# Optimization experiments

Measured on AMD Instinct MI355X. Metric: run time of the kernel, lower is better.

The kernel has to match this reference:

```python
import jax, jax.numpy as jnp
import numpy as np

B, T, D, H = 2, 2048, 768, 12
HS = D // H


def setup_inputs() -> dict:
    key = jax.random.key(0)
    ks = jax.random.split(key, 11)
    s = 1.0 / np.sqrt(D)
    return {
        "query": jax.random.normal(ks[0], (B, T, D), jnp.float32),
        "key": jax.random.normal(ks[1], (B, T, D), jnp.float32),
        "value": jax.random.normal(ks[2], (B, T, D), jnp.float32),
        "Wq": jax.random.normal(ks[3], (D, D), jnp.float32) * s,
        "bq": jax.random.normal(ks[4], (D,), jnp.float32) * s,
        "Wk": jax.random.normal(ks[5], (D, D), jnp.float32) * s,
        "bk": jax.random.normal(ks[6], (D,), jnp.float32) * s,
        "Wv": jax.random.normal(ks[7], (D, D), jnp.float32) * s,
        "bv": jax.random.normal(ks[8], (D,), jnp.float32) * s,
        "Wo": jax.random.normal(ks[9], (D, D), jnp.float32) * s,
        "bo": jax.random.normal(ks[10], (D,), jnp.float32) * s,
    }


def reference(query, key, value, Wq, bq, Wk, bk, Wv, bv, Wo, bo):
    # Projections (torch nn.Linear: x @ W.T + b), then split heads -> [B,H,T,HS]
    def split_heads(x):
        return x.reshape(B, -1, H, HS).transpose(0, 2, 1, 3)

    q = split_heads(query @ Wq.T + bq)
    k = split_heads(key @ Wk.T + bk)
    v = split_heads(value @ Wv.T + bv)

    scale = 1.0 / jnp.sqrt(jnp.asarray(HS, q.dtype))
    scores = jnp.einsum("bhqd,bhkd->bhqk", q, k) * scale  # [B,H,Tq,Tk]
    attn = jax.nn.softmax(scores, axis=-1)
    out = jnp.einsum("bhqk,bhkd->bhqd", attn, v)  # [B,H,Tq,HS]
    out = out.transpose(0, 2, 1, 3).reshape(B, -1, D)
    output = out @ Wo.T + bo
    return output, attn.mean(axis=1)
```

## Files before the change

### kernel.cpp

```cpp
#include <hip/hip_runtime.h>
#include <hip/hip_fp16.h>
#include <stdint.h>

typedef _Float16 f16;
typedef _Float16 f16x8 __attribute__((ext_vector_type(8)));
typedef _Float16 f16x4v __attribute__((ext_vector_type(4)));
typedef __fp16 h16x2 __attribute__((ext_vector_type(2)));
typedef float f32x4 __attribute__((ext_vector_type(4)));
typedef float f32x16 __attribute__((ext_vector_type(16)));

#define MFMA32(a,b,c) __builtin_amdgcn_mfma_f32_32x32x16_f16(a,b,c,0,0,0)
#define CVTPK(a,b) __builtin_amdgcn_cvt_pkrtz(a,b)

#if __has_builtin(__builtin_amdgcn_exp2f)
#define EXP2(x) __builtin_amdgcn_exp2f(x)
#else
#define EXP2(x) exp2f(x)
#endif

static __device__ __forceinline__ float dot2acc(h16x2 a, float c) {
#if __has_builtin(__builtin_amdgcn_fdot2)
    const h16x2 one = { (__fp16)1.f, (__fp16)1.f };
    return __builtin_amdgcn_fdot2(a, one, c, false);
#else
    return c + (float)a[0] + (float)a[1];
#endif
}

typedef __attribute__((address_space(1))) void gvoid_t;
typedef __attribute__((address_space(3))) void svoid_t;
#define AS1(p) ((gvoid_t*)(uintptr_t)(p))
#define AS3(p) ((svoid_t*)(uint32_t)(uintptr_t)(p))

static constexpr int Bc = 2, Tc = 2048, Dc = 768, Hc = 12;
static constexpr int Mc = Bc * Tc;
static constexpr float SC2 = 0.18033688011112042f;

union PA { f16x8 v; h16x2 h[4]; };

#define FRAG32(BASE, ROWOFF, CHUNK) \
    (*(const f16x8*)((const char*)(BASE) + \
        ((ROWOFF) + q32) * 128 + (((CHUNK) ^ g7) * 16)))

#define FRAGP(BASE, ROWOFF, C) \
    (*(const f16x8*)((const char*)(BASE) + \
        (((ROWOFF) / 2 + (q32 >> 1)) * 128) + \
        (((((q32 & 1) << 2) | (C)) ^ ((q32 >> 1) & 7)) * 16)))

__global__ __launch_bounds__(256) void conv_all(
    const float* __restrict__ q, const float* __restrict__ k, const float* __restrict__ v,
    const float* __restrict__ wq, const float* __restrict__ wk, const float* __restrict__ wv,
    const float* __restrict__ wo,
    f16* __restrict__ qh, f16* __restrict__ kh, f16* __restrict__ vh,
    f16* __restrict__ wqh, f16* __restrict__ wkh, f16* __restrict__ wvh, f16* __restrict__ woh)
{
    const int NI = (Mc * Dc) / 4;
    const int NW = (Dc * Dc) / 4;
    int i = blockIdx.x * 256 + threadIdx.x;
    if (i >= 3 * NI + 4 * NW) return;
    const float4* src; f16* dst; int j; float scl = 1.f;
    if (i < 3 * NI) {
        int a = i / NI; j = i - a * NI;
        src = (const float4*)(a == 0 ? q : (a == 1 ? k : v));
        dst = (a == 0 ? qh : (a == 1 ? kh : vh));
    } else {
        int t = i - 3 * NI;
        int a = t / NW; j = t - a * NW;
        src = (const float4*)(a == 0 ? wq : (a == 1 ? wk : (a == 2 ? wv : wo)));
        dst = (a == 0 ? wqh : (a == 1 ? wkh : (a == 2 ? wvh : woh)));
        if (a == 0) scl = SC2;
    }
    float4 f = src[j];
    f16x4v o = { (f16)(f.x * scl), (f16)(f.y * scl), (f16)(f.z * scl), (f16)(f.w * scl) };
    *(f16x4v*)(dst + 4 * j) = o;
}

__device__ __forceinline__ void gemm_bk32(
    const f16* __restrict__ A, const f16* __restrict__ W,
    int brow, int bcol, char* As, char* Bs, f32x16 acc[2])
{
    const int tid = threadIdx.x;
    const int w = tid >> 6, lane = tid & 63;
    const int q32 = lane & 31, hi = lane >> 5;
    const int wr = w >> 1, wc = w & 1;
    const int wbase16 = (tid & ~63) * 16;

#define GSA(KT_, BUF_) do { \
    const int k0_ = (KT_) * 32; \
    _Pragma("unroll") \
    for (int j_ = 0; j_ < 2; ++j_) { \
        const int p_ = j_ * 256 + tid; \
        const int L_ = p_ >> 3, c8_ = (p_ & 7) ^ (L_ & 7); \
        const int row_ = 2 * L_ + (c8_ >> 2), kc_ = (c8_ & 3) * 8; \
        __builtin_amdgcn_global_load_lds(AS1(A + (size_t)(brow + row_) * 768 + k0_ + kc_), \
            AS3(As + (BUF_) * 8192 + j_ * 4096 + wbase16), 16, 0, 0); \
    } } while (0)
#define GSB(KT_, BUF_) do { \
    const int k0_ = (KT_) * 32; \
    const int L_ = tid >> 3, c8_ = (tid & 7) ^ (L_ & 7); \
    const int row_ = 2 * L_ + (c8_ >> 2), kc_ = (c8_ & 3) * 8; \
    __builtin_amdgcn_global_load_lds(AS1(W + (size_t)(bcol + row_) * 768 + k0_ + kc_), \
        AS3(Bs + (BUF_) * 4096 + wbase16), 16, 0, 0); \
    } while (0)

    GSA(0, 0); GSB(0, 0);
    __syncthreads();
    for (int kt = 0; kt < 24; ++kt) {
        const int cur = kt & 1;
        if (kt < 23) { GSA(kt + 1, cur ^ 1); GSB(kt + 1, cur ^ 1); }
        const char* As_ = As + cur * 8192;
        const char* Bs_ = Bs + cur * 4096;
#pragma unroll
        for (int ks = 0; ks < 2; ++ks) {
            const f16x8 af0 = FRAGP(As_, wr * 64,      ks * 2 + hi);
            const f16x8 af1 = FRAGP(As_, wr * 64 + 32, ks * 2 + hi);
            const f16x8 bf  = FRAGP(Bs_, wc * 32,      ks * 2 + hi);
            acc[0] = MFMA32(af0, bf, acc[0]);
            acc[1] = MFMA32(af1, bf, acc[1]);
        }
        __syncthreads();
    }
#undef GSA
#undef GSB
}

__global__ __launch_bounds__(256) void qkv_proj(
    const f16* __restrict__ qh, const f16* __restrict__ kh, const f16* __restrict__ vh,
    const f16* __restrict__ wqh, const f16* __restrict__ wkh, const f16* __restrict__ wvh,
    const float* __restrict__ bq, const float* __restrict__ bk, const float* __restrict__ bv,
    f16* __restrict__ Qp, f16* __restrict__ Kp, f16* __restrict__ Vt)
{
    __shared__ char lds[24576];
    char* As = lds; char* Bs = lds + 16384;

    const int z = blockIdx.z;
    const f16* A = (z == 0) ? qh : (z == 1) ? kh : vh;
    const f16* W = (z == 0) ? wqh : (z == 1) ? wkh : wvh;
    const float* bias = (z == 0) ? bq : (z == 1) ? bk : bv;
    const int brow = blockIdx.y * 128, bcol = blockIdx.x * 64;

    f32x16 acc[2];
#pragma unroll
    for (int mi = 0; mi < 2; ++mi)
#pragma unroll
        for (int r = 0; r < 16; ++r) acc[mi][r] = 0.f;

    gemm_bk32(A, W, brow, bcol, As, Bs, acc);

    const int tid = threadIdx.x, w = tid >> 6, lane = tid & 63;
    const int q32 = lane & 31, hi = lane >> 5;
    const int wr = w >> 1, wc = w & 1;
    const int c = bcol + wc * 32 + q32;
    const float bval = (z == 0) ? bias[c] * SC2 : bias[c];

    if (z < 2) {
        f16* dst = (z == 0) ? Qp : Kp;
#pragma unroll
        for (int mi = 0; mi < 2; ++mi)
#pragma unroll
            for (int r = 0; r < 16; ++r) {
                const int row = brow + wr * 64 + mi * 32 + (r & 3) + 8 * (r >> 2) + 4 * hi;
                dst[(size_t)row * 768 + c] = (f16)(acc[mi][r] + bval);
            }
    } else {
        __syncthreads();
        const int dl = wc * 32 + q32;
#pragma unroll
        for (int mi = 0; mi < 2; ++mi)
#pragma unroll
            for (int j = 0; j < 8; ++j) {
                const int r0 = 2 * j;
                const int crow = (r0 & 3) + 8 * (r0 >> 2) + 4 * hi;
                const int sw = ((crow >> 2) ^ (crow >> 3)) & 1;
                const int tp = crow ^ (sw * 12);
                const int tloc = wr * 64 + mi * 32 + tp;
                const h16x2 pv = CVTPK(acc[mi][r0] + bval, acc[mi][r0 + 1] + bval);
                *(h16x2*)(As + dl * 256 + ((tloc * 2) ^ ((dl & 7) << 4))) = pv;
            }
        __syncthreads();
        const int bb = brow >> 11, t0 = brow & 2047, hh = bcol >> 6;
        f16* Vh = Vt + ((size_t)(bb * 12 + hh) * 64) * 2048;
#pragma unroll
        for (int j = 0; j < 4; ++j) {
            const int dr = j * 16 + (tid >> 4), off = tid & 15;
            const f16x8 vv = *(const f16x8*)(As + dr * 256 + ((off * 16) ^ ((dr & 7) << 4)));
            *(f16x8*)(Vh + (size_t)dr * 2048 + t0 + off * 8) = vv;
        }
    }
}

__global__ __launch_bounds__(256, 3) void attn_out(
    const f16* __restrict__ Qp, const f16* __restrict__ Kp, const f16* __restrict__ Vt,
    float* __restrict__ l_inv, f16* __restrict__ ctx)
{
    __shared__ f16 Kbuf[2][4096];
    __shared__ f16 Vbuf[2][4096];
    __shared__ float Ored[2][32][64];
    __shared__ float lred[2][2][32];

    const int qt = blockIdx.x, h = blockIdx.y, b = blockIdx.z;
    const int tid = threadIdx.x, w = tid >> 6, lane = tid & 63;
    const int q32 = lane & 31, hi = lane >> 5, g7 = lane & 7;
    const int qh = w & 1, kh = w >> 1;
    const int wbase16 = (tid & ~63) * 16;

    const size_t qrow0 = (size_t)b * 2048 + qt * 64 + qh * 32;
    const int hcol = h * 64;

    const f16* qb = Qp + (qrow0 + q32) * 768 + hcol + hi * 8;
    f16x8 bqf[4];
#pragma unroll
    for (int d = 0; d < 4; ++d) bqf[d] = *(const f16x8*)(qb + d * 16);

    const size_t kbase = (size_t)b * 2048;
    const f16* Vg = Vt + ((size_t)(b * 12 + h)) * 64 * 2048;

    f32x16 oacc[2];
#pragma unroll
    for (int dt = 0; dt < 2; ++dt)
#pragma unroll
        for (int r = 0; r < 16; ++r) oacc[dt][r] = 0.f;
    float lsum = 0.f;

#define STAGE_KV(KT_, BUF) do { \
    _Pragma("unroll") \
    for (int j_ = 0; j_ < 2; ++j_) { \
        const int p_ = j_ * 256 + tid; \
        const int row_ = p_ >> 3, c_ = (p_ & 7) ^ (row_ & 7); \
        __builtin_amdgcn_global_load_lds( \
            AS1(Kp + (kbase + (size_t)(KT_) * 64 + row_) * 768 + hcol + c_ * 8), \
            AS3((char*)&Kbuf[BUF][0] + j_ * 4096 + wbase16), 16, 0, 0); \
        __builtin_amdgcn_global_load_lds( \
            AS1(Vg + (size_t)row_ * 2048 + (KT_) * 64 + c_ * 8), \
            AS3((char*)&Vbuf[BUF][0] + j_ * 4096 + wbase16), 16, 0, 0); \
    } } while (0)

#define AOBODY(CUR) do { \
    const f16* Kb_ = &Kbuf[CUR][0]; const f16* Vb_ = &Vbuf[CUR][0]; \
    f32x16 sa; \
    _Pragma("unroll") \
    for (int r_ = 0; r_ < 16; ++r_) sa[r_] = 0.f; \
    sa = MFMA32(FRAG32(Kb_, kh * 32, 0 + hi), bqf[0], sa); \
    sa = MFMA32(FRAG32(Kb_, kh * 32, 2 + hi), bqf[1], sa); \
    sa = MFMA32(FRAG32(Kb_, kh * 32, 4 + hi), bqf[2], sa); \
    sa = MFMA32(FRAG32(Kb_, kh * 32, 6 + hi), bqf[3], sa); \
    float p[16]; \
    _Pragma("unroll") \
    for (int r_ = 0; r_ < 16; ++r_) p[r_] = EXP2(sa[r_]); \
    PA pa0, pa1; \
    pa0.h[0] = CVTPK(p[0], p[1]);   pa0.h[1] = CVTPK(p[2], p[3]); \
    pa0.h[2] = CVTPK(p[4], p[5]);   pa0.h[3] = CVTPK(p[6], p[7]); \
    pa1.h[0] = CVTPK(p[8], p[9]);   pa1.h[1] = CVTPK(p[10], p[11]); \
    pa1.h[2] = CVTPK(p[12], p[13]); pa1.h[3] = CVTPK(p[14], p[15]); \
    float t0_ = 0.f, t1_ = 0.f; \
    t0_ = dot2acc(pa0.h[0], t0_); t0_ = dot2acc(pa0.h[1], t0_); \
    t0_ = dot2acc(pa0.h[2], t0_); t0_ = dot2acc(pa0.h[3], t0_); \
    t1_ = dot2acc(pa1.h[0], t1_); t1_ = dot2acc(pa1.h[1], t1_); \
    t1_ = dot2acc(pa1.h[2], t1_); t1_ = dot2acc(pa1.h[3], t1_); \
    lsum += t0_ + t1_; \
    oacc[0] = MFMA32(FRAG32(Vb_, 0,  kh * 4 + 0 + hi), pa0.v, oacc[0]); \
    oacc[0] = MFMA32(FRAG32(Vb_, 0,  kh * 4 + 2 + hi), pa1.v, oacc[0]); \
    oacc[1] = MFMA32(FRAG32(Vb_, 32, kh * 4 + 0 + hi), pa0.v, oacc[1]); \
    oacc[1] = MFMA32(FRAG32(Vb_, 32, kh * 4 + 2 + hi), pa1.v, oacc[1]); \
} while (0)

    STAGE_KV(0, 0);
    __syncthreads();
    for (int kt = 0; kt < 32; ++kt) {
        const int cur = kt & 1;
        if (kt < 31) STAGE_KV(kt + 1, cur ^ 1);
        AOBODY(cur);
        __syncthreads();
    }
#undef STAGE_KV
#undef AOBODY

    lsum += __shfl_xor(lsum, 32);
    if (hi == 0) lred[kh][qh][q32] = lsum;
    if (kh == 1) {
#pragma unroll
        for (int dt = 0; dt < 2; ++dt)
#pragma unroll
            for (int g = 0; g < 4; ++g) {
                float4 v4 = { oacc[dt][g * 4 + 0], oacc[dt][g * 4 + 1],
                              oacc[dt][g * 4 + 2], oacc[dt][g * 4 + 3] };
                *(float4*)&Ored[qh][q32][dt * 32 + g * 8 + hi * 4] = v4;
            }
    }
    __syncthreads();
    if (kh == 0) {
        const float iv = 1.f / (lred[0][qh][q32] + lred[1][qh][q32]);
        if (hi == 0)
            l_inv[((size_t)(b * 12 + h)) * 2048 + qt * 64 + qh * 32 + q32] = iv;
        f16* cb = ctx + (qrow0 + q32) * 768 + hcol;
#pragma unroll
        for (int dt = 0; dt < 2; ++dt)
#pragma unroll
            for (int g = 0; g < 4; ++g) {
                const int d0 = dt * 32 + g * 8 + hi * 4;
                const float4 o4 = *(const float4*)&Ored[qh][q32][d0];
                f16x4v s;
#pragma unroll
                for (int e = 0; e < 4; ++e)
                    s[e] = (f16)((oacc[dt][g * 4 + e] + (&o4.x)[e]) * iv);
                *(f16x4v*)(cb + d0) = s;
            }
    }
}

__global__ __launch_bounds__(256) void tail_fused(
    const f16* __restrict__ ctx, const f16* __restrict__ woh,
    const float* __restrict__ bo, float* __restrict__ out,
    const f16* __restrict__ Qp, const f16* __restrict__ Kp,
    const float* __restrict__ l_inv, float* __restrict__ om)
{
    __shared__ char sh[32768];

    const int tid = threadIdx.x, w = tid >> 6, lane = tid & 63;
    const int q32 = lane & 31, hi = lane >> 5, g7 = lane & 7;
    const int wbase16 = (tid & ~63) * 16;

    if (blockIdx.x < 384) {
        const int brow = (blockIdx.x / 12) * 128, bcol = (blockIdx.x % 12) * 64;
        f32x16 acc[2];
#pragma unroll
        for (int mi = 0; mi < 2; ++mi)
#pragma unroll
            for (int r = 0; r < 16; ++r) acc[mi][r] = 0.f;

        gemm_bk32(ctx, woh, brow, bcol, sh, sh + 16384, acc);

        const int wr = w >> 1, wc = w & 1;
        const int c = bcol + wc * 32 + q32;
        const float bval = bo[c];
#pragma unroll
        for (int mi = 0; mi < 2; ++mi)
#pragma unroll
            for (int r = 0; r < 16; ++r) {
                const int row = brow + wr * 64 + mi * 32 + (r & 3) + 8 * (r >> 2) + 4 * hi;
                out[(size_t)row * 768 + c] = acc[mi][r] + bval;
            }
    } else {
        const int mb = blockIdx.x - 384;
        const int kt = mb & 31, r2 = mb >> 5;
        const int qt = r2 & 31, b = r2 >> 5;
        const int qh = w & 1, kh = w >> 1;

        char* Qb = sh;
        char* Kb = sh + 16384;

        const size_t qtrow = (size_t)b * 2048 + qt * 64;
        const size_t ktrow = (size_t)b * 2048 + kt * 64;

        f32x16 macc;
#pragma unroll
        for (int r = 0; r < 16; ++r) macc[r] = 0.f;

#define MSTAGE(H_, BUF) do { \
    _Pragma("unroll") \
    for (int j_ = 0; j_ < 2; ++j_) { \
        const int p_ = j_ * 256 + tid; \
        const int row_ = p_ >> 3, c_ = (p_ & 7) ^ (row_ & 7); \
        __builtin_amdgcn_global_load_lds( \
            AS1(Qp + (qtrow + row_) * 768 + (H_) * 64 + c_ * 8), \
            AS3(Qb + (BUF) * 8192 + j_ * 4096 + wbase16), 16, 0, 0); \
        __builtin_amdgcn_global_load_lds( \
            AS1(Kp + (ktrow + row_) * 768 + (H_) * 64 + c_ * 8), \
            AS3(Kb + (BUF) * 8192 + j_ * 4096 + wbase16), 16, 0, 0); \
    } } while (0)

#define MBODY(H_, CUR) do { \
    const f16* Qb_ = (const f16*)(Qb + (CUR) * 8192); \
    const f16* Kb_ = (const f16*)(Kb + (CUR) * 8192); \
    f16x8 qf[4]; \
    _Pragma("unroll") \
    for (int d_ = 0; d_ < 4; ++d_) qf[d_] = FRAG32(Qb_, qh * 32, d_ * 2 + hi); \
    f32x16 sa; \
    _Pragma("unroll") \
    for (int r_ = 0; r_ < 16; ++r_) sa[r_] = 0.f; \
    sa = MFMA32(FRAG32(Kb_, kh * 32, 0 + hi), qf[0], sa); \
    sa = MFMA32(FRAG32(Kb_, kh * 32, 2 + hi), qf[1], sa); \
    sa = MFMA32(FRAG32(Kb_, kh * 32, 4 + hi), qf[2], sa); \
    sa = MFMA32(FRAG32(Kb_, kh * 32, 6 + hi), qf[3], sa); \
    const float ivv = l_inv[((size_t)(b * 12 + (H_))) * 2048 + qt * 64 + qh * 32 + q32]; \
    _Pragma("unroll") \
    for (int r_ = 0; r_ < 16; ++r_) macc[r_] += EXP2(sa[r_]) * ivv; \
} while (0)

        MSTAGE(0, 0);
        __syncthreads();
        for (int h = 0; h < 12; ++h) {
            const int cur = h & 1;
            if (h < 11) MSTAGE(h + 1, cur ^ 1);
            MBODY(h, cur);
            __syncthreads();
        }
#undef MSTAGE
#undef MBODY

        float* ob = om + ((size_t)(b * 2048 + qt * 64 + qh * 32 + q32)) * 2048
                  + kt * 64 + kh * 32;
#pragma unroll
        for (int g = 0; g < 4; ++g) {
            float4 v4 = { macc[g * 4 + 0] * (1.0f / 12.0f),
                          macc[g * 4 + 1] * (1.0f / 12.0f),
                          macc[g * 4 + 2] * (1.0f / 12.0f),
                          macc[g * 4 + 3] * (1.0f / 12.0f) };
            *(float4*)(ob + g * 8 + hi * 4) = v4;
        }
    }
}

extern "C" void kernel_launch(void* const* d_in, const int* in_sizes, int n_in,
                              void* d_out, int out_size, void* d_ws, size_t ws_size,
                              hipStream_t stream) {
    const float* q  = (const float*)d_in[0];
    const float* k  = (const float*)d_in[1];
    const float* v  = (const float*)d_in[2];
    const float* Wq = (const float*)d_in[3];
    const float* bq = (const float*)d_in[4];
    const float* Wk = (const float*)d_in[5];
    const float* bk = (const float*)d_in[6];
    const float* Wv = (const float*)d_in[7];
    const float* bv = (const float*)d_in[8];
    const float* Wo = (const float*)d_in[9];
    const float* bo = (const float*)d_in[10];
    float* out = (float*)d_out;

    char* ws = (char*)d_ws;
    const size_t SZ_IN = (size_t)Mc * Dc * 2;
    const size_t SZ_W  = (size_t)Dc * Dc * 2;
    f16* qh  = (f16*)(ws);
    f16* kh  = (f16*)(ws + SZ_IN);
    f16* vh  = (f16*)(ws + 2 * SZ_IN);
    f16* wqh = (f16*)(ws + 3 * SZ_IN);
    f16* wkh = (f16*)(ws + 3 * SZ_IN + SZ_W);
    f16* wvh = (f16*)(ws + 3 * SZ_IN + 2 * SZ_W);
    f16* woh = (f16*)(ws + 3 * SZ_IN + 3 * SZ_W);
    f16* Qp  = (f16*)(ws + 3 * SZ_IN + 4 * SZ_W);
    f16* Kp  = (f16*)(ws + 4 * SZ_IN + 4 * SZ_W);
    f16* Vt  = (f16*)(ws + 5 * SZ_IN + 4 * SZ_W);
    f16* ctx = qh;
    float* l_inv = (float*)kh;

    conv_all<<<dim3(11520), dim3(256), 0, stream>>>(q, k, v, Wq, Wk, Wv, Wo,
                                                    qh, kh, vh, wqh, wkh, wvh, woh);
    qkv_proj<<<dim3(12, 32, 3), dim3(256), 0, stream>>>(qh, kh, vh, wqh, wkh, wvh,
                                                        bq, bk, bv, Qp, Kp, Vt);
    attn_out<<<dim3(32, 12, 2), dim3(256), 0, stream>>>(Qp, Kp, Vt, l_inv, ctx);
    tail_fused<<<dim3(2432), dim3(256), 0, stream>>>(ctx, woh, bo, out,
                                                     Qp, Kp, l_inv,
                                                     out + (size_t)Mc * Dc);
}
```

Measured before the change: 130.0 us.

## Fuse fp32-to-fp16 conversion into GEMM loaders, drop separate conversion kernel

The standalone conversion kernel that cast inputs and weights to fp16 is removed. The QKV projection GEMM now loads fp32 activations and weights into registers, converts them (applying the Q scale to Wq), and writes fp16 tiles to LDS. The output-projection GEMM does the same for Wo while still streaming ctx through direct global-to-LDS loads. This saves a kernel launch and the extra global write and read of fp16 copies. In exchange, each block reads twice the bytes per tile, weights are converted redundantly across blocks, and register-staged loads replace the async LDS path.

```diff
diff --git a/kernel.cpp b/kernel.cpp
--- a/kernel.cpp
+++ b/kernel.cpp
@@ -47,36 +47,9 @@
         (((ROWOFF) / 2 + (q32 >> 1)) * 128) + \
         (((((q32 & 1) << 2) | (C)) ^ ((q32 >> 1) & 7)) * 16)))
 
-__global__ __launch_bounds__(256) void conv_all(
-    const float* __restrict__ q, const float* __restrict__ k, const float* __restrict__ v,
-    const float* __restrict__ wq, const float* __restrict__ wk, const float* __restrict__ wv,
-    const float* __restrict__ wo,
-    f16* __restrict__ qh, f16* __restrict__ kh, f16* __restrict__ vh,
-    f16* __restrict__ wqh, f16* __restrict__ wkh, f16* __restrict__ wvh, f16* __restrict__ woh)
-{
-    const int NI = (Mc * Dc) / 4;
-    const int NW = (Dc * Dc) / 4;
-    int i = blockIdx.x * 256 + threadIdx.x;
-    if (i >= 3 * NI + 4 * NW) return;
-    const float4* src; f16* dst; int j; float scl = 1.f;
-    if (i < 3 * NI) {
-        int a = i / NI; j = i - a * NI;
-        src = (const float4*)(a == 0 ? q : (a == 1 ? k : v));
-        dst = (a == 0 ? qh : (a == 1 ? kh : vh));
-    } else {
-        int t = i - 3 * NI;
-        int a = t / NW; j = t - a * NW;
-        src = (const float4*)(a == 0 ? wq : (a == 1 ? wk : (a == 2 ? wv : wo)));
-        dst = (a == 0 ? wqh : (a == 1 ? wkh : (a == 2 ? wvh : woh)));
-        if (a == 0) scl = SC2;
-    }
-    float4 f = src[j];
-    f16x4v o = { (f16)(f.x * scl), (f16)(f.y * scl), (f16)(f.z * scl), (f16)(f.w * scl) };
-    *(f16x4v*)(dst + 4 * j) = o;
-}
-
-__device__ __forceinline__ void gemm_bk32(
-    const f16* __restrict__ A, const f16* __restrict__ W,
+template<bool AF32>
+__device__ __forceinline__ void gemm_bk32_t(
+    const void* Av, const float* __restrict__ W, float wscl,
     int brow, int bcol, char* As, char* Bs, f32x16 acc[2])
 {
     const int tid = threadIdx.x;
@@ -85,48 +58,89 @@
     const int wr = w >> 1, wc = w & 1;
     const int wbase16 = (tid & ~63) * 16;
 
-#define GSA(KT_, BUF_) do { \
-    const int k0_ = (KT_) * 32; \
+    int arow[2], akc[2];
+#pragma unroll
+    for (int j = 0; j < 2; ++j) {
+        const int p = j * 256 + tid;
+        const int L = p >> 3, c8 = (p & 7) ^ (L & 7);
+        arow[j] = 2 * L + (c8 >> 2); akc[j] = (c8 & 3) * 8;
+    }
+    const int bL = tid >> 3, bc8 = (tid & 7) ^ (bL & 7);
+    const int browW = 2 * bL + (bc8 >> 2), bkc = (bc8 & 3) * 8;
+
+    float4 af[2][2], bw[2];
+
+#define LOADW(KT_) do { \
+    const float* wp_ = W + (size_t)(bcol + browW) * 768 + (KT_) * 32 + bkc; \
+    bw[0] = *(const float4*)(wp_); bw[1] = *(const float4*)(wp_ + 4); } while (0)
+
+#define LOADA(KT_) do { \
     _Pragma("unroll") \
     for (int j_ = 0; j_ < 2; ++j_) { \
-        const int p_ = j_ * 256 + tid; \
-        const int L_ = p_ >> 3, c8_ = (p_ & 7) ^ (L_ & 7); \
-        const int row_ = 2 * L_ + (c8_ >> 2), kc_ = (c8_ & 3) * 8; \
-        __builtin_amdgcn_global_load_lds(AS1(A + (size_t)(brow + row_) * 768 + k0_ + kc_), \
-            AS3(As + (BUF_) * 8192 + j_ * 4096 + wbase16), 16, 0, 0); \
-    } } while (0)
-#define GSB(KT_, BUF_) do { \
-    const int k0_ = (KT_) * 32; \
-    const int L_ = tid >> 3, c8_ = (tid & 7) ^ (L_ & 7); \
-    const int row_ = 2 * L_ + (c8_ >> 2), kc_ = (c8_ & 3) * 8; \
-    __builtin_amdgcn_global_load_lds(AS1(W + (size_t)(bcol + row_) * 768 + k0_ + kc_), \
-        AS3(Bs + (BUF_) * 4096 + wbase16), 16, 0, 0); \
-    } while (0)
-
-    GSA(0, 0); GSB(0, 0);
+        const float* ap_ = (const float*)Av + (size_t)(brow + arow[j_]) * 768 + (KT_) * 32 + akc[j_]; \
+        af[j_][0] = *(const float4*)(ap_); af[j_][1] = *(const float4*)(ap_ + 4); } } while (0)
+
+#define GLDSA(KT_, BUF_) do { \
+    _Pragma("unroll") \
+    for (int j_ = 0; j_ < 2; ++j_) \
+        __builtin_amdgcn_global_load_lds( \
+            AS1((const f16*)Av + (size_t)(brow + arow[j_]) * 768 + (KT_) * 32 + akc[j_]), \
+            AS3(As + (BUF_) * 8192 + j_ * 4096 + wbase16), 16, 0, 0); } while (0)
+
+#define WRITEW(BUF_) do { \
+    f16x8 o_; \
+    _Pragma("unroll") \
+    for (int e_ = 0; e_ < 4; ++e_) o_[e_] = (f16)((&bw[0].x)[e_] * wscl); \
+    _Pragma("unroll") \
+    for (int e_ = 0; e_ < 4; ++e_) o_[4 + e_] = (f16)((&bw[1].x)[e_] * wscl); \
+    *(f16x8*)(Bs + (BUF_) * 4096 + tid * 16) = o_; } while (0)
+
+#define WRITEA(BUF_) do { \
+    _Pragma("unroll") \
+    for (int j_ = 0; j_ < 2; ++j_) { \
+        f16x8 o_; \
+        _Pragma("unroll") \
+        for (int e_ = 0; e_ < 4; ++e_) o_[e_] = (f16)((&af[j_][0].x)[e_]); \
+        _Pragma("unroll") \
+        for (int e_ = 0; e_ < 4; ++e_) o_[4 + e_] = (f16)((&af[j_][1].x)[e_]); \
+        *(f16x8*)(As + (BUF_) * 8192 + j_ * 4096 + tid * 16) = o_; } } while (0)
+
+    LOADW(0);
+    if constexpr (AF32) { LOADA(0); WRITEA(0); } else { GLDSA(0, 0); }
+    WRITEW(0);
     __syncthreads();
     for (int kt = 0; kt < 24; ++kt) {
         const int cur = kt & 1;
-        if (kt < 23) { GSA(kt + 1, cur ^ 1); GSB(kt + 1, cur ^ 1); }
+        if (kt < 23) {
+            LOADW(kt + 1);
+            if constexpr (AF32) LOADA(kt + 1); else GLDSA(kt + 1, cur ^ 1);
+        }
         const char* As_ = As + cur * 8192;
         const char* Bs_ = Bs + cur * 4096;
 #pragma unroll
         for (int ks = 0; ks < 2; ++ks) {
-            const f16x8 af0 = FRAGP(As_, wr * 64,      ks * 2 + hi);
-            const f16x8 af1 = FRAGP(As_, wr * 64 + 32, ks * 2 + hi);
-            const f16x8 bf  = FRAGP(Bs_, wc * 32,      ks * 2 + hi);
-            acc[0] = MFMA32(af0, bf, acc[0]);
-            acc[1] = MFMA32(af1, bf, acc[1]);
+            const f16x8 a0 = FRAGP(As_, wr * 64,      ks * 2 + hi);
+            const f16x8 a1 = FRAGP(As_, wr * 64 + 32, ks * 2 + hi);
+            const f16x8 bb = FRAGP(Bs_, wc * 32,      ks * 2 + hi);
+            acc[0] = MFMA32(a0, bb, acc[0]);
+            acc[1] = MFMA32(a1, bb, acc[1]);
+        }
+        if (kt < 23) {
+            if constexpr (AF32) WRITEA(cur ^ 1);
+            WRITEW(cur ^ 1);
         }
         __syncthreads();
     }
-#undef GSA
-#undef GSB
+#undef LOADW
+#undef LOADA
+#undef GLDSA
+#undef WRITEW
+#undef WRITEA
 }
 
 __global__ __launch_bounds__(256) void qkv_proj(
-    const f16* __restrict__ qh, const f16* __restrict__ kh, const f16* __restrict__ vh,
-    const f16* __restrict__ wqh, const f16* __restrict__ wkh, const f16* __restrict__ wvh,
+    const float* __restrict__ q, const float* __restrict__ k, const float* __restrict__ v,
+    const float* __restrict__ Wq, const float* __restrict__ Wk, const float* __restrict__ Wv,
     const float* __restrict__ bq, const float* __restrict__ bk, const float* __restrict__ bv,
     f16* __restrict__ Qp, f16* __restrict__ Kp, f16* __restrict__ Vt)
 {
@@ -134,9 +148,10 @@
     char* As = lds; char* Bs = lds + 16384;
 
     const int z = blockIdx.z;
-    const f16* A = (z == 0) ? qh : (z == 1) ? kh : vh;
-    const f16* W = (z == 0) ? wqh : (z == 1) ? wkh : wvh;
+    const float* A = (z == 0) ? q : (z == 1) ? k : v;
+    const float* W = (z == 0) ? Wq : (z == 1) ? Wk : Wv;
     const float* bias = (z == 0) ? bq : (z == 1) ? bk : bv;
+    const float wscl = (z == 0) ? SC2 : 1.f;
     const int brow = blockIdx.y * 128, bcol = blockIdx.x * 64;
 
     f32x16 acc[2];
@@ -145,7 +160,7 @@
 #pragma unroll
         for (int r = 0; r < 16; ++r) acc[mi][r] = 0.f;
 
-    gemm_bk32(A, W, brow, bcol, As, Bs, acc);
+    gemm_bk32_t<true>(A, W, wscl, brow, bcol, As, Bs, acc);
 
     const int tid = threadIdx.x, w = tid >> 6, lane = tid & 63;
     const int q32 = lane & 31, hi = lane >> 5;
@@ -309,7 +324,7 @@
 }
 
 __global__ __launch_bounds__(256) void tail_fused(
-    const f16* __restrict__ ctx, const f16* __restrict__ woh,
+    const f16* __restrict__ ctx, const float* __restrict__ Wo,
     const float* __restrict__ bo, float* __restrict__ out,
     const f16* __restrict__ Qp, const f16* __restrict__ Kp,
     const float* __restrict__ l_inv, float* __restrict__ om)
@@ -328,7 +343,7 @@
 #pragma unroll
             for (int r = 0; r < 16; ++r) acc[mi][r] = 0.f;
 
-        gemm_bk32(ctx, woh, brow, bcol, sh, sh + 16384, acc);
+        gemm_bk32_t<false>(ctx, Wo, 1.f, brow, bcol, sh, sh + 16384, acc);
 
         const int wr = w >> 1, wc = w & 1;
         const int c = bcol + wc * 32 + q32;
@@ -429,26 +444,16 @@
 
     char* ws = (char*)d_ws;
     const size_t SZ_IN = (size_t)Mc * Dc * 2;
-    const size_t SZ_W  = (size_t)Dc * Dc * 2;
-    f16* qh  = (f16*)(ws);
-    f16* kh  = (f16*)(ws + SZ_IN);
-    f16* vh  = (f16*)(ws + 2 * SZ_IN);
-    f16* wqh = (f16*)(ws + 3 * SZ_IN);
-    f16* wkh = (f16*)(ws + 3 * SZ_IN + SZ_W);
-    f16* wvh = (f16*)(ws + 3 * SZ_IN + 2 * SZ_W);
-    f16* woh = (f16*)(ws + 3 * SZ_IN + 3 * SZ_W);
-    f16* Qp  = (f16*)(ws + 3 * SZ_IN + 4 * SZ_W);
-    f16* Kp  = (f16*)(ws + 4 * SZ_IN + 4 * SZ_W);
-    f16* Vt  = (f16*)(ws + 5 * SZ_IN + 4 * SZ_W);
-    f16* ctx = qh;
-    float* l_inv = (float*)kh;
-
-    conv_all<<<dim3(11520), dim3(256), 0, stream>>>(q, k, v, Wq, Wk, Wv, Wo,
-                                                    qh, kh, vh, wqh, wkh, wvh, woh);
-    qkv_proj<<<dim3(12, 32, 3), dim3(256), 0, stream>>>(qh, kh, vh, wqh, wkh, wvh,
+    f16* ctx   = (f16*)(ws);
+    float* l_inv = (float*)(ws + SZ_IN);
+    f16* Qp    = (f16*)(ws + 2 * SZ_IN);
+    f16* Kp    = (f16*)(ws + 3 * SZ_IN);
+    f16* Vt    = (f16*)(ws + 4 * SZ_IN);
+
+    qkv_proj<<<dim3(12, 32, 3), dim3(256), 0, stream>>>(q, k, v, Wq, Wk, Wv,
                                                         bq, bk, bv, Qp, Kp, Vt);
     attn_out<<<dim3(32, 12, 2), dim3(256), 0, stream>>>(Qp, Kp, Vt, l_inv, ctx);
-    tail_fused<<<dim3(2432), dim3(256), 0, stream>>>(ctx, woh, bo, out,
+    tail_fused<<<dim3(2432), dim3(256), 0, stream>>>(ctx, Wo, bo, out,
                                                      Qp, Kp, l_inv,
                                                      out + (size_t)Mc * Dc);
 }
```

Measured after the change: 136.8 us. 1.05x slower.

## Alias attention LDS buffers, raise occupancy to 4 waves, unroll KV loop by two

Applied to the files above, without the earlier changes.

Shared memory for the K/V double buffers and the final O/l reduction scratch is merged into one arena, and the reduction arrays alias the K/V buffers, so per-block LDS drops to about 33 KB. Launch bounds rise from 3 to 4 blocks per CU to use the freed LDS. The KV loop is unrolled by two so buffer indices are compile-time constants rather than computed from kt parity. The higher occupancy target may force the compiler to cap registers and spill, and the aliasing is only safe because a barrier separates the last AOBODY from the reduction writes.

```diff
diff --git a/kernel.cpp b/kernel.cpp
--- a/kernel.cpp
+++ b/kernel.cpp
@@ -189,14 +189,18 @@
     }
 }
 
-__global__ __launch_bounds__(256, 3) void attn_out(
+__global__ __launch_bounds__(256, 4) void attn_out(
     const f16* __restrict__ Qp, const f16* __restrict__ Kp, const f16* __restrict__ Vt,
     float* __restrict__ l_inv, f16* __restrict__ ctx)
 {
-    __shared__ f16 Kbuf[2][4096];
-    __shared__ f16 Vbuf[2][4096];
-    __shared__ float Ored[2][32][64];
-    __shared__ float lred[2][2][32];
+    __shared__ char arena[33280];
+
+    f16* Kbuf0 = (f16*)(arena);
+    f16* Kbuf1 = (f16*)(arena + 8192);
+    f16* Vbuf0 = (f16*)(arena + 16384);
+    f16* Vbuf1 = (f16*)(arena + 24576);
+    float (*Ored)[32][64] = (float (*)[32][64])(arena);
+    float (*lred)[2][32]  = (float (*)[2][32])(arena + 16384);
 
     const int qt = blockIdx.x, h = blockIdx.y, b = blockIdx.z;
     const int tid = threadIdx.x, w = tid >> 6, lane = tid & 63;
@@ -222,21 +226,21 @@
         for (int r = 0; r < 16; ++r) oacc[dt][r] = 0.f;
     float lsum = 0.f;
 
-#define STAGE_KV(KT_, BUF) do { \
+#define STAGE_KV(KT_, KB_, VB_) do { \
     _Pragma("unroll") \
     for (int j_ = 0; j_ < 2; ++j_) { \
         const int p_ = j_ * 256 + tid; \
         const int row_ = p_ >> 3, c_ = (p_ & 7) ^ (row_ & 7); \
         __builtin_amdgcn_global_load_lds( \
             AS1(Kp + (kbase + (size_t)(KT_) * 64 + row_) * 768 + hcol + c_ * 8), \
-            AS3((char*)&Kbuf[BUF][0] + j_ * 4096 + wbase16), 16, 0, 0); \
+            AS3((char*)(KB_) + j_ * 4096 + wbase16), 16, 0, 0); \
         __builtin_amdgcn_global_load_lds( \
             AS1(Vg + (size_t)row_ * 2048 + (KT_) * 64 + c_ * 8), \
-            AS3((char*)&Vbuf[BUF][0] + j_ * 4096 + wbase16), 16, 0, 0); \
+            AS3((char*)(VB_) + j_ * 4096 + wbase16), 16, 0, 0); \
     } } while (0)
 
-#define AOBODY(CUR) do { \
-    const f16* Kb_ = &Kbuf[CUR][0]; const f16* Vb_ = &Vbuf[CUR][0]; \
+#define AOBODY(KB_, VB_) do { \
+    const f16* Kb_ = (KB_); const f16* Vb_ = (VB_); \
     f32x16 sa; \
     _Pragma("unroll") \
     for (int r_ = 0; r_ < 16; ++r_) sa[r_] = 0.f; \
@@ -264,12 +268,14 @@
     oacc[1] = MFMA32(FRAG32(Vb_, 32, kh * 4 + 2 + hi), pa1.v, oacc[1]); \
 } while (0)
 
-    STAGE_KV(0, 0);
+    STAGE_KV(0, Kbuf0, Vbuf0);
     __syncthreads();
-    for (int kt = 0; kt < 32; ++kt) {
-        const int cur = kt & 1;
-        if (kt < 31) STAGE_KV(kt + 1, cur ^ 1);
-        AOBODY(cur);
+    for (int kt = 0; kt < 32; kt += 2) {
+        STAGE_KV(kt + 1, Kbuf1, Vbuf1);
+        AOBODY(Kbuf0, Vbuf0);
+        __syncthreads();
+        if (kt < 30) STAGE_KV(kt + 2, Kbuf0, Vbuf0);
+        AOBODY(Kbuf1, Vbuf1);
         __syncthreads();
     }
 #undef STAGE_KV
```

After: 130.7 us. About the same (+0.5%).
